# Optimization experiments

Hardware: AMD Instinct MI355X
Metric: run time of the kernel (lower is better)

Reference implementation:

```python
import jax, jax.numpy as jnp
import numpy as np

N_HEADS = 8
EPS = 1e-6


def setup_inputs() -> dict:
    key = jax.random.key(0)
    k1, k2, k3, k4, k5 = jax.random.split(key, 5)
    C_in, C_out = 512, 512
    x = jax.random.normal(k1, (4, C_in, 128, 128), dtype=jnp.float32)
    # Linear layers: torch stores weight as (out, in); init ~ U(-1/sqrt(in), 1/sqrt(in))
    s_in = 1.0 / np.sqrt(C_in)
    w_qkv = jax.random.uniform(k2, (3 * C_in, C_in), minval=-s_in, maxval=s_in, dtype=jnp.float32)
    b_qkv = jax.random.uniform(k3, (3 * C_in,), minval=-s_in, maxval=s_in, dtype=jnp.float32)
    w_out = jax.random.uniform(k4, (C_out, C_in), minval=-s_in, maxval=s_in, dtype=jnp.float32)
    b_out = jax.random.uniform(k5, (C_out,), minval=-s_in, maxval=s_in, dtype=jnp.float32)
    return {"x": x, "w_qkv": w_qkv, "b_qkv": b_qkv, "w_out": w_out, "b_out": b_out}


def reference(x, w_qkv, b_qkv, w_out, b_out):
    B, C = x.shape[0], x.shape[1]
    spatial = x.shape[2:]
    c = C // N_HEADS  # channels per head
    # features_last=False: move channels to last, flatten spatial -> (B, N, C)
    xl = jnp.moveaxis(x, 1, -1).reshape(B, -1, C)
    N = xl.shape[1]
    qkv = xl @ w_qkv.T + b_qkv  # (B, N, 3*C)
    # einops '(qkv head channels)': qkv outermost, then head, then channels
    qkv = qkv.reshape(B, N, 3, N_HEADS, c)
    q = jax.nn.relu(qkv[:, :, 0])  # (B, N, H, c)
    k = jax.nn.relu(qkv[:, :, 1])
    v = qkv[:, :, 2]
    # Associativity: value @ key^T @ query == value @ (key^T @ query).
    # kq[b,h,c,d] = sum_n k[b,n,h,c] * q[b,n,h,d]  -> small (c x c) per head
    kq = jnp.einsum('bnhc,bnhd->bhcd', k, q)
    vkq = jnp.einsum('bnhc,bhcd->bnhd', v, kq)  # (B, N, H, c)
    # Padded ones-row of value corresponds to column-sum of kq over axis c
    norm = kq.sum(axis=2)[:, None] + EPS  # (B, 1, H, c)
    attn = vkq / norm  # (B, N, H, c)
    # torch: (B,H,N,c).moveaxis(1,-1) -> (B,N,c,H); flatten(-2) -> (B,N,c*H)
    attn = jnp.transpose(attn, (0, 1, 3, 2)).reshape(B, N, -1)
    out = attn @ w_out.T + b_out  # (B, N, C_out)
    out = out.reshape(B, *spatial, -1)
    out = jnp.moveaxis(out, -1, 1)  # (B, C_out, *spatial)
    return out
```

## Files before the change

kernel.cpp:

```cpp
#include <hip/hip_runtime.h>
#include <hip/hip_bf16.h>
#include <stdint.h>

#define NSP 16384
#define BATCH 4
#define EPSV 1e-6f

typedef __attribute__((ext_vector_type(8))) short fragAB;
typedef __attribute__((ext_vector_type(4))) float fragC;

__device__ __forceinline__ unsigned short f2bf(float f) {
    union { float f; unsigned u; } un; un.f = f;
    unsigned r = un.u + 0x7fffu + ((un.u >> 16) & 1u);
    return (unsigned short)(r >> 16);
}

#define GLD_LDS(g, l) __builtin_amdgcn_global_load_lds( \
    (const __attribute__((address_space(1))) void*)(g), \
    (__attribute__((address_space(3))) void*)(l), 16, 0, 0)

__device__ __forceinline__ fragAB ldfrag(const unsigned short* ls, int m, int g) {
    return *(const fragAB*)&ls[((m >> 3) << 9) + ((m & 7) << 6) + ((g ^ (m & 7)) << 3)];
}

__device__ __forceinline__ int tidx(int ch, int g) {
    return (ch << 7) + ((g ^ (ch & 7)) << 3);
}

__global__ __launch_bounds__(256) void transpose_x(const float* __restrict__ x,
                                                   unsigned short* __restrict__ xt) {
    __shared__ float lds[64 * 65];
    const int b  = blockIdx.z;
    const int c0 = blockIdx.y * 64;
    const int n0 = blockIdx.x * 64;
    const int t  = threadIdx.x;
    const int nl = (t & 15) * 4;
    const int cl = t >> 4;
#pragma unroll
    for (int i = 0; i < 4; ++i) {
        int c = cl + i * 16;
        float4 v = *(const float4*)&x[((size_t)(b * 512 + c0 + c)) * NSP + n0 + nl];
        float* row = &lds[c * 65 + nl];
        row[0] = v.x; row[1] = v.y; row[2] = v.z; row[3] = v.w;
    }
    __syncthreads();
#pragma unroll
    for (int i = 0; i < 2; ++i) {
        int ch = t + i * 256;
        int n  = ch >> 3;
        int co = (ch & 7) * 8;
        unsigned v0, v1, v2, v3;
        v0 = f2bf(lds[(co + 0) * 65 + n]) | ((unsigned)f2bf(lds[(co + 1) * 65 + n]) << 16);
        v1 = f2bf(lds[(co + 2) * 65 + n]) | ((unsigned)f2bf(lds[(co + 3) * 65 + n]) << 16);
        v2 = f2bf(lds[(co + 4) * 65 + n]) | ((unsigned)f2bf(lds[(co + 5) * 65 + n]) << 16);
        v3 = f2bf(lds[(co + 6) * 65 + n]) | ((unsigned)f2bf(lds[(co + 7) * 65 + n]) << 16);
        uint4 pk; pk.x = v0; pk.y = v1; pk.z = v2; pk.w = v3;
        *(uint4*)&xt[((size_t)(b * NSP + n0 + n)) * 512 + c0 + co] = pk;
    }
}

__global__ __launch_bounds__(256) void prep(const float* __restrict__ wqkv,
                                            unsigned short* __restrict__ wqb,
                                            unsigned short* __restrict__ wvT) {
    __shared__ float lds[64 * 65];
    const int blk = blockIdx.x;
    const int t   = threadIdx.x;
    if (blk < 512) {
        int i = (blk * 256 + t) * 4;
        float4 v = *(const float4*)&wqkv[i];
        uint2 pk;
        pk.x = f2bf(v.x) | ((unsigned)f2bf(v.y) << 16);
        pk.y = f2bf(v.z) | ((unsigned)f2bf(v.w) << 16);
        *(uint2*)&wqb[i] = pk;
        return;
    }
    const int c0  = ((blk - 512) & 7) * 64;
    const int ch0 = ((blk - 512) >> 3) * 64;
    const int cl  = (t & 15) * 4;
    const int rl  = t >> 4;
#pragma unroll
    for (int i = 0; i < 4; ++i) {
        int r = rl + i * 16;
        float4 v = *(const float4*)&wqkv[((size_t)(1024 + ch0 + r)) * 512 + c0 + cl];
        float* row = &lds[r * 65 + cl];
        row[0] = v.x; row[1] = v.y; row[2] = v.z; row[3] = v.w;
    }
    __syncthreads();
#pragma unroll
    for (int i = 0; i < 2; ++i) {
        int idx = t + i * 256;
        int c = idx >> 3;
        int g = (idx & 7) * 8;
        unsigned v0, v1, v2, v3;
        v0 = f2bf(lds[(g + 0) * 65 + c]) | ((unsigned)f2bf(lds[(g + 1) * 65 + c]) << 16);
        v1 = f2bf(lds[(g + 2) * 65 + c]) | ((unsigned)f2bf(lds[(g + 3) * 65 + c]) << 16);
        v2 = f2bf(lds[(g + 4) * 65 + c]) | ((unsigned)f2bf(lds[(g + 5) * 65 + c]) << 16);
        v3 = f2bf(lds[(g + 6) * 65 + c]) | ((unsigned)f2bf(lds[(g + 7) * 65 + c]) << 16);
        uint4 pk; pk.x = v0; pk.y = v1; pk.z = v2; pk.w = v3;
        *(uint4*)&wvT[((size_t)(c0 + c)) * 512 + ch0 + g] = pk;
    }
}

__global__ __launch_bounds__(256, 2) void gemm_qk_kq(
    const unsigned short* __restrict__ xt, const unsigned short* __restrict__ wq,
    const float* __restrict__ bqkv, float* __restrict__ part) {
    __shared__ unsigned short S[(128 + 256) * 64];
    __shared__ unsigned short Qt[128 * 128];
    unsigned short* Bls = &S[8192];
    unsigned short* Kt  = &S[0];

    const int b  = blockIdx.z;
    const int hc = blockIdx.y;
    const int bx = blockIdx.x;
    const int n0 = bx * 128;
    const int t  = threadIdx.x;
    const int wv = t >> 6, ln = t & 63;
    const unsigned short* Ag = xt + (size_t)(b * NSP + n0) * 512;
    const int srow = ln >> 3;
    const int scol = ((ln & 7) ^ srow) << 3;
    const int isK = wv >> 1;
    unsigned short* T = isK ? Kt : Qt;

    fragC acc[8][4];
#pragma unroll
    for (int i = 0; i < 8; ++i)
#pragma unroll
        for (int j = 0; j < 4; ++j) { acc[i][j][0]=0.f; acc[i][j][1]=0.f; acc[i][j][2]=0.f; acc[i][j][3]=0.f; }

    for (int k0 = 0; k0 < 512; k0 += 64) {
#pragma unroll
        for (int i = 0; i < 4; ++i) {
            int ca = wv * 4 + i;
            GLD_LDS(Ag + (size_t)(ca * 8 + srow) * 512 + k0 + scol, &S[ca * 512]);
        }
#pragma unroll
        for (int i = 0; i < 8; ++i) {
            int cb = wv * 8 + i;
            int jl = cb * 8 + srow;
            int rg = hc * 128 + jl + ((jl & 128) ? 384 : 0);
            GLD_LDS(wq + (size_t)rg * 512 + k0 + scol, &Bls[cb * 512]);
        }
        __syncthreads();
#pragma unroll
        for (int kk = 0; kk < 64; kk += 32) {
            int g = (kk >> 3) + (ln >> 4);
            fragAB bf[4];
#pragma unroll
            for (int nt = 0; nt < 4; ++nt) bf[nt] = ldfrag(Bls, wv * 64 + nt * 16 + (ln & 15), g);
#pragma unroll
            for (int mt = 0; mt < 8; ++mt) {
                fragAB a = ldfrag(S, mt * 16 + (ln & 15), g);
#pragma unroll
                for (int nt = 0; nt < 4; ++nt)
                    acc[mt][nt] = __builtin_amdgcn_mfma_f32_16x16x32_bf16(a, bf[nt], acc[mt][nt], 0, 0, 0);
            }
        }
        __syncthreads();
    }

#pragma unroll
    for (int nt = 0; nt < 4; ++nt) {
        int chl = (wv & 1) * 64 + nt * 16 + (ln & 15);
        float bias = bqkv[hc * 128 + chl + (isK ? 512 : 0)];
#pragma unroll
        for (int mt = 0; mt < 8; ++mt) {
            int nb = mt * 16 + (ln >> 4) * 4;
            float r0 = acc[mt][nt][0] + bias; r0 = r0 > 0.f ? r0 : 0.f;
            float r1 = acc[mt][nt][1] + bias; r1 = r1 > 0.f ? r1 : 0.f;
            float r2 = acc[mt][nt][2] + bias; r2 = r2 > 0.f ? r2 : 0.f;
            float r3 = acc[mt][nt][3] + bias; r3 = r3 > 0.f ? r3 : 0.f;
            uint2 pk;
            pk.x = f2bf(r0) | ((unsigned)f2bf(r1) << 16);
            pk.y = f2bf(r2) | ((unsigned)f2bf(r3) << 16);
            int g = nb >> 3, o = nb & 7;
            *(uint2*)&T[tidx(chl, g) + o] = pk;
        }
    }
    __syncthreads();

    {
        const int wm = wv >> 1, wn = wv & 1;
        fragC ak[4][2];
#pragma unroll
        for (int i = 0; i < 4; ++i)
#pragma unroll
            for (int j = 0; j < 2; ++j) { ak[i][j][0]=0.f; ak[i][j][1]=0.f; ak[i][j][2]=0.f; ak[i][j][3]=0.f; }
        const int dh = wn * 32;
#pragma unroll
        for (int kk = 0; kk < 128; kk += 32) {
            int g = (kk >> 3) + (ln >> 4);
            fragAB bq[2];
#pragma unroll
            for (int dt = 0; dt < 2; ++dt)
                bq[dt] = *(const fragAB*)&Qt[tidx(wm * 64 + dh + dt * 16 + (ln & 15), g)];
#pragma unroll
            for (int mt = 0; mt < 4; ++mt) {
                fragAB a = *(const fragAB*)&Kt[tidx(wm * 64 + mt * 16 + (ln & 15), g)];
#pragma unroll
                for (int dt = 0; dt < 2; ++dt)
                    ak[mt][dt] = __builtin_amdgcn_mfma_f32_16x16x32_bf16(a, bq[dt], ak[mt][dt], 0, 0, 0);
            }
        }
        float* pb = part + ((size_t)((b * 8 + hc * 2 + wm) * 128 + bx)) * 4096;
#pragma unroll
        for (int mt = 0; mt < 4; ++mt)
#pragma unroll
            for (int dt = 0; dt < 2; ++dt) {
                int d = dh + dt * 16 + (ln & 15);
#pragma unroll
                for (int r = 0; r < 4; ++r) {
                    int c = mt * 16 + (ln >> 4) * 4 + r;
                    pb[c * 64 + d] = ak[mt][dt][r];
                }
            }
    }
}

__global__ __launch_bounds__(256) void reduce_kq(const float* __restrict__ part,
                                                 float* __restrict__ kq) {
    const int tid = blockIdx.x * 256 + threadIdx.x;
    const int bh  = tid >> 10;
    const int e4  = tid & 1023;
    const float4* p = (const float4*)part + (size_t)bh * 128 * 1024 + e4;
    float4 s0 = {0.f, 0.f, 0.f, 0.f}, s1 = {0.f, 0.f, 0.f, 0.f};
#pragma unroll 4
    for (int blk = 0; blk < 128; blk += 2) {
        float4 v0 = p[(size_t)blk * 1024];
        float4 v1 = p[(size_t)(blk + 1) * 1024];
        s0.x += v0.x; s0.y += v0.y; s0.z += v0.z; s0.w += v0.w;
        s1.x += v1.x; s1.y += v1.y; s1.z += v1.z; s1.w += v1.w;
    }
    float4 s; s.x = s0.x + s1.x; s.y = s0.y + s1.y; s.z = s0.z + s1.z; s.w = s0.w + s1.w;
    ((float4*)kq)[(size_t)bh * 1024 + e4] = s;
}

__global__ __launch_bounds__(256) void w2_kernel(
    const float* __restrict__ kq, const float* __restrict__ wout,
    const float* __restrict__ bqkv,
    unsigned short* __restrict__ W2, float* __restrict__ bias2acc) {
    __shared__ float slab[64 * 65];
    __shared__ float part[4 * 64];
    __shared__ float rnorm[64];
    __shared__ float wsc[32 * 65];
    const int jc = blockIdx.x;
    const int h  = blockIdx.y;
    const int b  = blockIdx.z;
    const int t  = threadIdx.x;
    const float* kqb = kq + ((size_t)(b * 8 + h)) * 4096;
#pragma unroll
    for (int i = 0; i < 4; ++i) {
        int e = t * 16 + i * 4;
        float4 v = *(const float4*)&kqb[e];
        float* r = &slab[(e >> 6) * 65 + (e & 63)];
        r[0] = v.x; r[1] = v.y; r[2] = v.z; r[3] = v.w;
    }
    __syncthreads();
    {
        int d = t & 63, cq = t >> 6;
        float s = 0.f;
        for (int c = cq * 16; c < cq * 16 + 16; ++c) s += slab[c * 65 + d];
        part[cq * 64 + d] = s;
    }
    __syncthreads();
    if (t < 64) rnorm[t] = 1.0f / (part[t] + part[64 + t] + part[128 + t] + part[192 + t] + EPSV);
    __syncthreads();
    {
        int jl = t >> 3;
        const float* wrow = &wout[((size_t)(jc * 32 + jl)) * 512 + h];
#pragma unroll
        for (int i = 0; i < 8; ++i) {
            int d = (t & 7) * 8 + i;
            wsc[jl * 65 + d] = wrow[d * 8] * rnorm[d];
        }
    }
    __syncthreads();
    {
        int jl = t >> 3, cg = (t & 7) * 8;
        int j  = jc * 32 + jl;
        float a[8] = {0.f, 0.f, 0.f, 0.f, 0.f, 0.f, 0.f, 0.f};
        for (int d = 0; d < 64; ++d) {
            float w = wsc[jl * 65 + d];
#pragma unroll
            for (int i = 0; i < 8; ++i) a[i] += w * slab[(cg + i) * 65 + d];
        }
        uint4 pk;
        pk.x = f2bf(a[0]) | ((unsigned)f2bf(a[1]) << 16);
        pk.y = f2bf(a[2]) | ((unsigned)f2bf(a[3]) << 16);
        pk.z = f2bf(a[4]) | ((unsigned)f2bf(a[5]) << 16);
        pk.w = f2bf(a[6]) | ((unsigned)f2bf(a[7]) << 16);
        *(uint4*)&W2[((size_t)(b * 512 + j)) * 512 + h * 64 + cg] = pk;
        const float* bv = &bqkv[1024 + h * 64 + cg];
        float p = 0.f;
#pragma unroll
        for (int i = 0; i < 8; ++i) p += a[i] * bv[i];
        p += __shfl_down(p, 4, 64);
        p += __shfl_down(p, 2, 64);
        p += __shfl_down(p, 1, 64);
        if ((t & 7) == 0) atomicAdd(&bias2acc[b * 512 + j], p);
    }
}

__global__ __launch_bounds__(256) void w3_kernel(
    const unsigned short* __restrict__ wvT, const unsigned short* __restrict__ W2,
    unsigned short* __restrict__ W3) {
    __shared__ unsigned short Als[128 * 64];
    __shared__ unsigned short Bls[128 * 64];
    const int b  = blockIdx.z;
    const int m0 = blockIdx.x * 128;
    const int n0 = blockIdx.y * 128;
    const int t  = threadIdx.x;
    const int wv = t >> 6, ln = t & 63;
    const unsigned short* Ag = wvT + (size_t)m0 * 512;
    const unsigned short* Bg = W2 + ((size_t)(b * 512 + n0)) * 512;

    fragC acc[4][4];
#pragma unroll
    for (int i = 0; i < 4; ++i)
#pragma unroll
        for (int j = 0; j < 4; ++j) { acc[i][j][0]=0.f; acc[i][j][1]=0.f; acc[i][j][2]=0.f; acc[i][j][3]=0.f; }

    const int mw = (wv >> 1) * 64, nw = (wv & 1) * 64;
    const int srow = ln >> 3;
    const int scol = ((ln & 7) ^ srow) << 3;

    for (int k0 = 0; k0 < 512; k0 += 64) {
#pragma unroll
        for (int i = 0; i < 4; ++i) {
            int chunk = wv * 4 + i;
            int row = chunk * 8 + srow;
            GLD_LDS(Ag + (size_t)row * 512 + k0 + scol, &Als[chunk * 512]);
            GLD_LDS(Bg + (size_t)row * 512 + k0 + scol, &Bls[chunk * 512]);
        }
        __syncthreads();
#pragma unroll
        for (int kk = 0; kk < 64; kk += 32) {
            int g = (kk >> 3) + (ln >> 4);
            fragAB a[4], bf[4];
#pragma unroll
            for (int mt = 0; mt < 4; ++mt) a[mt]  = ldfrag(Als, mw + mt * 16 + (ln & 15), g);
#pragma unroll
            for (int nt = 0; nt < 4; ++nt) bf[nt] = ldfrag(Bls, nw + nt * 16 + (ln & 15), g);
#pragma unroll
            for (int mt = 0; mt < 4; ++mt)
#pragma unroll
                for (int nt = 0; nt < 4; ++nt)
                    acc[mt][nt] = __builtin_amdgcn_mfma_f32_16x16x32_bf16(a[mt], bf[nt], acc[mt][nt], 0, 0, 0);
        }
        __syncthreads();
    }

#pragma unroll
    for (int mt = 0; mt < 4; ++mt)
#pragma unroll
        for (int nt = 0; nt < 4; ++nt) {
            int c = m0 + mw + mt * 16 + (ln >> 4) * 4;
            int j = n0 + nw + nt * 16 + (ln & 15);
            uint2 pk;
            pk.x = f2bf(acc[mt][nt][0]) | ((unsigned)f2bf(acc[mt][nt][1]) << 16);
            pk.y = f2bf(acc[mt][nt][2]) | ((unsigned)f2bf(acc[mt][nt][3]) << 16);
            *(uint2*)&W3[((size_t)(b * 512 + j)) * 512 + c] = pk;
        }
}

__global__ __launch_bounds__(256, 2) void gemm_out(
    const unsigned short* __restrict__ xt, const unsigned short* __restrict__ W3,
    const float* __restrict__ bias2acc, const float* __restrict__ bout,
    float* __restrict__ out) {
    __shared__ unsigned short Als[128 * 64];
    __shared__ unsigned short Bls[256 * 64];
    const int b  = blockIdx.z;
    const int n0 = blockIdx.x * 128;
    const int j0 = blockIdx.y * 256;
    const int t  = threadIdx.x;
    const int wv = t >> 6, ln = t & 63;
    const unsigned short* Ag = xt + (size_t)(b * NSP + n0) * 512;
    const unsigned short* Bg = W3 + ((size_t)(b * 512 + j0)) * 512;

    fragC acc[8][4];
#pragma unroll
    for (int i = 0; i < 8; ++i)
#pragma unroll
        for (int j = 0; j < 4; ++j) { acc[i][j][0]=0.f; acc[i][j][1]=0.f; acc[i][j][2]=0.f; acc[i][j][3]=0.f; }

    const int srow = ln >> 3;
    const int scol = ((ln & 7) ^ srow) << 3;

    for (int k0 = 0; k0 < 512; k0 += 64) {
#pragma unroll
        for (int i = 0; i < 4; ++i) {
            int ca = wv * 4 + i;
            GLD_LDS(Ag + (size_t)(ca * 8 + srow) * 512 + k0 + scol, &Als[ca * 512]);
        }
#pragma unroll
        for (int i = 0; i < 8; ++i) {
            int cb = wv * 8 + i;
            GLD_LDS(Bg + (size_t)(cb * 8 + srow) * 512 + k0 + scol, &Bls[cb * 512]);
        }
        __syncthreads();
#pragma unroll
        for (int kk = 0; kk < 64; kk += 32) {
            int g = (kk >> 3) + (ln >> 4);
            fragAB bf[4];
#pragma unroll
            for (int nt = 0; nt < 4; ++nt) bf[nt] = ldfrag(Bls, wv * 64 + nt * 16 + (ln & 15), g);
#pragma unroll
            for (int mt = 0; mt < 8; ++mt) {
                fragAB a = ldfrag(Als, mt * 16 + (ln & 15), g);
#pragma unroll
                for (int nt = 0; nt < 4; ++nt)
                    acc[mt][nt] = __builtin_amdgcn_mfma_f32_16x16x32_bf16(a, bf[nt], acc[mt][nt], 0, 0, 0);
            }
        }
        __syncthreads();
    }

#pragma unroll
    for (int nt = 0; nt < 4; ++nt) {
        int j = j0 + wv * 64 + nt * 16 + (ln & 15);
        float bias = bout[j] + bias2acc[b * 512 + j];
#pragma unroll
        for (int mt = 0; mt < 8; ++mt) {
            int n = n0 + mt * 16 + (ln >> 4) * 4;
            float4 v;
            v.x = acc[mt][nt][0] + bias;
            v.y = acc[mt][nt][1] + bias;
            v.z = acc[mt][nt][2] + bias;
            v.w = acc[mt][nt][3] + bias;
            *(float4*)&out[((size_t)(b * 512 + j)) * NSP + n] = v;
        }
    }
}

extern "C" void kernel_launch(void* const* d_in, const int* in_sizes, int n_in,
                              void* d_out, int out_size, void* d_ws, size_t ws_size,
                              hipStream_t stream) {
    const float* x    = (const float*)d_in[0];
    const float* wqkv = (const float*)d_in[1];
    const float* bqkv = (const float*)d_in[2];
    const float* wout = (const float*)d_in[3];
    const float* bout = (const float*)d_in[4];
    float* out = (float*)d_out;

    char* p = (char*)d_ws;
    unsigned short* xt   = (unsigned short*)p; p += (size_t)BATCH * NSP * 512 * 2;
    unsigned short* wqb  = (unsigned short*)p; p += (size_t)1024 * 512 * 2;
    unsigned short* wvT  = (unsigned short*)p; p += (size_t)512 * 512 * 2;
    float*          part = (float*)p;          p += (size_t)32 * 128 * 4096 * 4;
    float*          kq   = (float*)p;          p += (size_t)BATCH * 32768 * 4;
    float*          b2a  = (float*)p;          p += (size_t)BATCH * 512 * 4;
    unsigned short* W2   = (unsigned short*)p; p += (size_t)BATCH * 512 * 512 * 2;
    unsigned short* W3   = (unsigned short*)p; p += (size_t)BATCH * 512 * 512 * 2;

    hipMemsetAsync(b2a, 0, (size_t)BATCH * 512 * 4, stream);
    transpose_x<<<dim3(256, 8, BATCH), 256, 0, stream>>>(x, xt);
    prep<<<dim3(576), 256, 0, stream>>>(wqkv, wqb, wvT);
    gemm_qk_kq<<<dim3(128, 4, BATCH), 256, 0, stream>>>(xt, wqb, bqkv, part);
    reduce_kq<<<dim3(128), 256, 0, stream>>>(part, kq);
    w2_kernel<<<dim3(16, 8, BATCH), 256, 0, stream>>>(kq, wout, bqkv, W2, b2a);
    w3_kernel<<<dim3(4, 4, BATCH), 256, 0, stream>>>(wvT, W2, W3);
    gemm_out<<<dim3(128, 2, BATCH), 256, 0, stream>>>(xt, W3, b2a, bout, out);
}
```

Before: 396.6 us.

## Fuse transpose with weight prep and W2 with W3 into single kernels

Merges the x transpose and weight-conversion kernels into one launch. It also fuses the per-head W2 computation with the W3 GEMM so W2 stays in shared memory and never goes to global memory. The bias accumulation becomes a direct store, which removes the memset and the atomics. The cost is that the fused W2/W3 kernel runs on only 64 blocks and reads wvT fragments straight from global memory with no LDS staging, so that stage may be latency-bound.

```diff
diff --git a/kernel.cpp b/kernel.cpp
--- a/kernel.cpp
+++ b/kernel.cpp
@@ -27,46 +27,45 @@
     return (ch << 7) + ((g ^ (ch & 7)) << 3);
 }
 
-__global__ __launch_bounds__(256) void transpose_x(const float* __restrict__ x,
-                                                   unsigned short* __restrict__ xt) {
-    __shared__ float lds[64 * 65];
-    const int b  = blockIdx.z;
-    const int c0 = blockIdx.y * 64;
-    const int n0 = blockIdx.x * 64;
-    const int t  = threadIdx.x;
-    const int nl = (t & 15) * 4;
-    const int cl = t >> 4;
-#pragma unroll
-    for (int i = 0; i < 4; ++i) {
-        int c = cl + i * 16;
-        float4 v = *(const float4*)&x[((size_t)(b * 512 + c0 + c)) * NSP + n0 + nl];
-        float* row = &lds[c * 65 + nl];
-        row[0] = v.x; row[1] = v.y; row[2] = v.z; row[3] = v.w;
-    }
-    __syncthreads();
-#pragma unroll
-    for (int i = 0; i < 2; ++i) {
-        int ch = t + i * 256;
-        int n  = ch >> 3;
-        int co = (ch & 7) * 8;
-        unsigned v0, v1, v2, v3;
-        v0 = f2bf(lds[(co + 0) * 65 + n]) | ((unsigned)f2bf(lds[(co + 1) * 65 + n]) << 16);
-        v1 = f2bf(lds[(co + 2) * 65 + n]) | ((unsigned)f2bf(lds[(co + 3) * 65 + n]) << 16);
-        v2 = f2bf(lds[(co + 4) * 65 + n]) | ((unsigned)f2bf(lds[(co + 5) * 65 + n]) << 16);
-        v3 = f2bf(lds[(co + 6) * 65 + n]) | ((unsigned)f2bf(lds[(co + 7) * 65 + n]) << 16);
-        uint4 pk; pk.x = v0; pk.y = v1; pk.z = v2; pk.w = v3;
-        *(uint4*)&xt[((size_t)(b * NSP + n0 + n)) * 512 + c0 + co] = pk;
-    }
-}
-
-__global__ __launch_bounds__(256) void prep(const float* __restrict__ wqkv,
-                                            unsigned short* __restrict__ wqb,
-                                            unsigned short* __restrict__ wvT) {
+__global__ __launch_bounds__(256) void transpose_prep(
+    const float* __restrict__ x, unsigned short* __restrict__ xt,
+    const float* __restrict__ wqkv, unsigned short* __restrict__ wqb,
+    unsigned short* __restrict__ wvT) {
     __shared__ float lds[64 * 65];
     const int blk = blockIdx.x;
     const int t   = threadIdx.x;
-    if (blk < 512) {
-        int i = (blk * 256 + t) * 4;
+    if (blk < 8192) {
+        const int b  = blk >> 11;
+        const int c0 = ((blk >> 8) & 7) * 64;
+        const int n0 = (blk & 255) * 64;
+        const int nl = (t & 15) * 4;
+        const int cl = t >> 4;
+#pragma unroll
+        for (int i = 0; i < 4; ++i) {
+            int c = cl + i * 16;
+            float4 v = *(const float4*)&x[((size_t)(b * 512 + c0 + c)) * NSP + n0 + nl];
+            float* row = &lds[c * 65 + nl];
+            row[0] = v.x; row[1] = v.y; row[2] = v.z; row[3] = v.w;
+        }
+        __syncthreads();
+#pragma unroll
+        for (int i = 0; i < 2; ++i) {
+            int ch = t + i * 256;
+            int n  = ch >> 3;
+            int co = (ch & 7) * 8;
+            unsigned v0, v1, v2, v3;
+            v0 = f2bf(lds[(co + 0) * 65 + n]) | ((unsigned)f2bf(lds[(co + 1) * 65 + n]) << 16);
+            v1 = f2bf(lds[(co + 2) * 65 + n]) | ((unsigned)f2bf(lds[(co + 3) * 65 + n]) << 16);
+            v2 = f2bf(lds[(co + 4) * 65 + n]) | ((unsigned)f2bf(lds[(co + 5) * 65 + n]) << 16);
+            v3 = f2bf(lds[(co + 6) * 65 + n]) | ((unsigned)f2bf(lds[(co + 7) * 65 + n]) << 16);
+            uint4 pk; pk.x = v0; pk.y = v1; pk.z = v2; pk.w = v3;
+            *(uint4*)&xt[((size_t)(b * NSP + n0 + n)) * 512 + c0 + co] = pk;
+        }
+        return;
+    }
+    const int pblk = blk - 8192;
+    if (pblk < 512) {
+        int i = (pblk * 256 + t) * 4;
         float4 v = *(const float4*)&wqkv[i];
         uint2 pk;
         pk.x = f2bf(v.x) | ((unsigned)f2bf(v.y) << 16);
@@ -74,8 +73,8 @@
         *(uint2*)&wqb[i] = pk;
         return;
     }
-    const int c0  = ((blk - 512) & 7) * 64;
-    const int ch0 = ((blk - 512) >> 3) * 64;
+    const int c0  = ((pblk - 512) & 7) * 64;
+    const int ch0 = ((pblk - 512) >> 3) * 64;
     const int cl  = (t & 15) * 4;
     const int rl  = t >> 4;
 #pragma unroll
@@ -234,132 +233,114 @@
     ((float4*)kq)[(size_t)bh * 1024 + e4] = s;
 }
 
-__global__ __launch_bounds__(256) void w2_kernel(
+__global__ __launch_bounds__(256) void w2w3(
     const float* __restrict__ kq, const float* __restrict__ wout,
-    const float* __restrict__ bqkv,
-    unsigned short* __restrict__ W2, float* __restrict__ bias2acc) {
+    const float* __restrict__ bqkv, const unsigned short* __restrict__ wvT,
+    unsigned short* __restrict__ W3, float* __restrict__ bias2acc) {
     __shared__ float slab[64 * 65];
-    __shared__ float part[4 * 64];
+    __shared__ float p4[4 * 64];
     __shared__ float rnorm[64];
     __shared__ float wsc[32 * 65];
+    __shared__ unsigned short W2loc[32 * 520];
     const int jc = blockIdx.x;
-    const int h  = blockIdx.y;
-    const int b  = blockIdx.z;
+    const int b  = blockIdx.y;
     const int t  = threadIdx.x;
-    const float* kqb = kq + ((size_t)(b * 8 + h)) * 4096;
-#pragma unroll
-    for (int i = 0; i < 4; ++i) {
-        int e = t * 16 + i * 4;
-        float4 v = *(const float4*)&kqb[e];
-        float* r = &slab[(e >> 6) * 65 + (e & 63)];
-        r[0] = v.x; r[1] = v.y; r[2] = v.z; r[3] = v.w;
-    }
-    __syncthreads();
+    const int jl = t >> 3, cg = (t & 7) * 8;
+    float pacc = 0.f;
+
+    for (int h = 0; h < 8; ++h) {
+        const float* kqb = kq + ((size_t)(b * 8 + h)) * 4096;
+#pragma unroll
+        for (int i = 0; i < 4; ++i) {
+            int e = t * 16 + i * 4;
+            float4 v = *(const float4*)&kqb[e];
+            float* r = &slab[(e >> 6) * 65 + (e & 63)];
+            r[0] = v.x; r[1] = v.y; r[2] = v.z; r[3] = v.w;
+        }
+        __syncthreads();
+        {
+            int d = t & 63, cq = t >> 6;
+            float s = 0.f;
+            for (int c = cq * 16; c < cq * 16 + 16; ++c) s += slab[c * 65 + d];
+            p4[cq * 64 + d] = s;
+        }
+        __syncthreads();
+        if (t < 64) rnorm[t] = 1.0f / (p4[t] + p4[64 + t] + p4[128 + t] + p4[192 + t] + EPSV);
+        __syncthreads();
+        {
+            const float* wrow = &wout[((size_t)(jc * 32 + jl)) * 512 + h];
+#pragma unroll
+            for (int i = 0; i < 8; ++i) {
+                int d = (t & 7) * 8 + i;
+                wsc[jl * 65 + d] = wrow[d * 8] * rnorm[d];
+            }
+        }
+        __syncthreads();
+        {
+            float a[8] = {0.f, 0.f, 0.f, 0.f, 0.f, 0.f, 0.f, 0.f};
+            for (int d = 0; d < 64; ++d) {
+                float w = wsc[jl * 65 + d];
+#pragma unroll
+                for (int i = 0; i < 8; ++i) a[i] += w * slab[(cg + i) * 65 + d];
+            }
+            uint4 pk;
+            pk.x = f2bf(a[0]) | ((unsigned)f2bf(a[1]) << 16);
+            pk.y = f2bf(a[2]) | ((unsigned)f2bf(a[3]) << 16);
+            pk.z = f2bf(a[4]) | ((unsigned)f2bf(a[5]) << 16);
+            pk.w = f2bf(a[6]) | ((unsigned)f2bf(a[7]) << 16);
+            *(uint4*)&W2loc[jl * 520 + h * 64 + cg] = pk;
+            const float* bv = &bqkv[1024 + h * 64 + cg];
+#pragma unroll
+            for (int i = 0; i < 8; ++i) pacc += a[i] * bv[i];
+        }
+        __syncthreads();
+    }
+
     {
-        int d = t & 63, cq = t >> 6;
-        float s = 0.f;
-        for (int c = cq * 16; c < cq * 16 + 16; ++c) s += slab[c * 65 + d];
-        part[cq * 64 + d] = s;
-    }
-    __syncthreads();
-    if (t < 64) rnorm[t] = 1.0f / (part[t] + part[64 + t] + part[128 + t] + part[192 + t] + EPSV);
-    __syncthreads();
-    {
-        int jl = t >> 3;
-        const float* wrow = &wout[((size_t)(jc * 32 + jl)) * 512 + h];
-#pragma unroll
-        for (int i = 0; i < 8; ++i) {
-            int d = (t & 7) * 8 + i;
-            wsc[jl * 65 + d] = wrow[d * 8] * rnorm[d];
-        }
-    }
-    __syncthreads();
-    {
-        int jl = t >> 3, cg = (t & 7) * 8;
-        int j  = jc * 32 + jl;
-        float a[8] = {0.f, 0.f, 0.f, 0.f, 0.f, 0.f, 0.f, 0.f};
-        for (int d = 0; d < 64; ++d) {
-            float w = wsc[jl * 65 + d];
-#pragma unroll
-            for (int i = 0; i < 8; ++i) a[i] += w * slab[(cg + i) * 65 + d];
-        }
-        uint4 pk;
-        pk.x = f2bf(a[0]) | ((unsigned)f2bf(a[1]) << 16);
-        pk.y = f2bf(a[2]) | ((unsigned)f2bf(a[3]) << 16);
-        pk.z = f2bf(a[4]) | ((unsigned)f2bf(a[5]) << 16);
-        pk.w = f2bf(a[6]) | ((unsigned)f2bf(a[7]) << 16);
-        *(uint4*)&W2[((size_t)(b * 512 + j)) * 512 + h * 64 + cg] = pk;
-        const float* bv = &bqkv[1024 + h * 64 + cg];
-        float p = 0.f;
-#pragma unroll
-        for (int i = 0; i < 8; ++i) p += a[i] * bv[i];
+        float p = pacc;
         p += __shfl_down(p, 4, 64);
         p += __shfl_down(p, 2, 64);
         p += __shfl_down(p, 1, 64);
-        if ((t & 7) == 0) atomicAdd(&bias2acc[b * 512 + j], p);
-    }
-}
-
-__global__ __launch_bounds__(256) void w3_kernel(
-    const unsigned short* __restrict__ wvT, const unsigned short* __restrict__ W2,
-    unsigned short* __restrict__ W3) {
-    __shared__ unsigned short Als[128 * 64];
-    __shared__ unsigned short Bls[128 * 64];
-    const int b  = blockIdx.z;
-    const int m0 = blockIdx.x * 128;
-    const int n0 = blockIdx.y * 128;
-    const int t  = threadIdx.x;
-    const int wv = t >> 6, ln = t & 63;
-    const unsigned short* Ag = wvT + (size_t)m0 * 512;
-    const unsigned short* Bg = W2 + ((size_t)(b * 512 + n0)) * 512;
-
-    fragC acc[4][4];
-#pragma unroll
-    for (int i = 0; i < 4; ++i)
-#pragma unroll
-        for (int j = 0; j < 4; ++j) { acc[i][j][0]=0.f; acc[i][j][1]=0.f; acc[i][j][2]=0.f; acc[i][j][3]=0.f; }
-
-    const int mw = (wv >> 1) * 64, nw = (wv & 1) * 64;
-    const int srow = ln >> 3;
-    const int scol = ((ln & 7) ^ srow) << 3;
-
-    for (int k0 = 0; k0 < 512; k0 += 64) {
-#pragma unroll
-        for (int i = 0; i < 4; ++i) {
-            int chunk = wv * 4 + i;
-            int row = chunk * 8 + srow;
-            GLD_LDS(Ag + (size_t)row * 512 + k0 + scol, &Als[chunk * 512]);
-            GLD_LDS(Bg + (size_t)row * 512 + k0 + scol, &Bls[chunk * 512]);
-        }
-        __syncthreads();
-#pragma unroll
-        for (int kk = 0; kk < 64; kk += 32) {
-            int g = (kk >> 3) + (ln >> 4);
-            fragAB a[4], bf[4];
-#pragma unroll
-            for (int mt = 0; mt < 4; ++mt) a[mt]  = ldfrag(Als, mw + mt * 16 + (ln & 15), g);
-#pragma unroll
-            for (int nt = 0; nt < 4; ++nt) bf[nt] = ldfrag(Bls, nw + nt * 16 + (ln & 15), g);
-#pragma unroll
-            for (int mt = 0; mt < 4; ++mt)
-#pragma unroll
-                for (int nt = 0; nt < 4; ++nt)
-                    acc[mt][nt] = __builtin_amdgcn_mfma_f32_16x16x32_bf16(a[mt], bf[nt], acc[mt][nt], 0, 0, 0);
-        }
-        __syncthreads();
-    }
-
-#pragma unroll
-    for (int mt = 0; mt < 4; ++mt)
-#pragma unroll
-        for (int nt = 0; nt < 4; ++nt) {
-            int c = m0 + mw + mt * 16 + (ln >> 4) * 4;
-            int j = n0 + nw + nt * 16 + (ln & 15);
-            uint2 pk;
-            pk.x = f2bf(acc[mt][nt][0]) | ((unsigned)f2bf(acc[mt][nt][1]) << 16);
-            pk.y = f2bf(acc[mt][nt][2]) | ((unsigned)f2bf(acc[mt][nt][3]) << 16);
-            *(uint2*)&W3[((size_t)(b * 512 + j)) * 512 + c] = pk;
-        }
+        if ((t & 7) == 0) bias2acc[b * 512 + jc * 32 + jl] = p;
+    }
+    __syncthreads();
+
+    {
+        const int wv = t >> 6, ln = t & 63;
+        const int c0w = wv * 128;
+        fragC acc[8][2];
+#pragma unroll
+        for (int i = 0; i < 8; ++i)
+#pragma unroll
+            for (int j = 0; j < 2; ++j) { acc[i][j][0]=0.f; acc[i][j][1]=0.f; acc[i][j][2]=0.f; acc[i][j][3]=0.f; }
+        for (int ks = 0; ks < 16; ++ks) {
+            int k0 = ks * 32;
+            int koff = k0 + (ln >> 4) * 8;
+            fragAB bw[2];
+#pragma unroll
+            for (int ni = 0; ni < 2; ++ni)
+                bw[ni] = *(const fragAB*)&W2loc[(ni * 16 + (ln & 15)) * 520 + koff];
+#pragma unroll
+            for (int mi = 0; mi < 8; ++mi) {
+                int c = c0w + mi * 16 + (ln & 15);
+                fragAB a = *(const fragAB*)&wvT[(size_t)c * 512 + koff];
+#pragma unroll
+                for (int ni = 0; ni < 2; ++ni)
+                    acc[mi][ni] = __builtin_amdgcn_mfma_f32_16x16x32_bf16(a, bw[ni], acc[mi][ni], 0, 0, 0);
+            }
+        }
+#pragma unroll
+        for (int mi = 0; mi < 8; ++mi)
+#pragma unroll
+            for (int ni = 0; ni < 2; ++ni) {
+                int c = c0w + mi * 16 + (ln >> 4) * 4;
+                int j = jc * 32 + ni * 16 + (ln & 15);
+                uint2 pk;
+                pk.x = f2bf(acc[mi][ni][0]) | ((unsigned)f2bf(acc[mi][ni][1]) << 16);
+                pk.y = f2bf(acc[mi][ni][2]) | ((unsigned)f2bf(acc[mi][ni][3]) << 16);
+                *(uint2*)&W3[((size_t)(b * 512 + j)) * 512 + c] = pk;
+            }
+    }
 }
 
 __global__ __launch_bounds__(256, 2) void gemm_out(
@@ -448,15 +429,11 @@
     float*          part = (float*)p;          p += (size_t)32 * 128 * 4096 * 4;
     float*          kq   = (float*)p;          p += (size_t)BATCH * 32768 * 4;
     float*          b2a  = (float*)p;          p += (size_t)BATCH * 512 * 4;
-    unsigned short* W2   = (unsigned short*)p; p += (size_t)BATCH * 512 * 512 * 2;
     unsigned short* W3   = (unsigned short*)p; p += (size_t)BATCH * 512 * 512 * 2;
 
-    hipMemsetAsync(b2a, 0, (size_t)BATCH * 512 * 4, stream);
-    transpose_x<<<dim3(256, 8, BATCH), 256, 0, stream>>>(x, xt);
-    prep<<<dim3(576), 256, 0, stream>>>(wqkv, wqb, wvT);
+    transpose_prep<<<dim3(8768), 256, 0, stream>>>(x, xt, wqkv, wqb, wvT);
     gemm_qk_kq<<<dim3(128, 4, BATCH), 256, 0, stream>>>(xt, wqb, bqkv, part);
     reduce_kq<<<dim3(128), 256, 0, stream>>>(part, kq);
-    w2_kernel<<<dim3(16, 8, BATCH), 256, 0, stream>>>(kq, wout, bqkv, W2, b2a);
-    w3_kernel<<<dim3(4, 4, BATCH), 256, 0, stream>>>(wvT, W2, W3);
+    w2w3<<<dim3(16, BATCH), 256, 0, stream>>>(kq, wout, bqkv, wvT, W3, b2a);
     gemm_out<<<dim3(128, 2, BATCH), 256, 0, stream>>>(xt, W3, b2a, bout, out);
 }
```

Result: slower. 445.1 us (+12.2%).
